# Kernel optimization log

Measured on AMD Instinct MI355X. Metric: run time of the kernel, lower is better.

## Reference

```python
import jax, jax.numpy as jnp
import numpy as np

B, S, E, D = 4, 4096, 512, 64

def setup_inputs() -> dict:
    key = jax.random.key(0)
    kx, kq, kk, kv = jax.random.split(key, 4)
    # xavier_normal std = sqrt(2/(E+D))
    std = float(np.sqrt(2.0 / (E + D)))
    return {
        "x": jax.random.normal(kx, (B, S, E), dtype=jnp.float32),
        "WQ": jax.random.normal(kq, (E, D), dtype=jnp.float32) * std,
        "WK": jax.random.normal(kk, (E, D), dtype=jnp.float32) * std,
        "WV": jax.random.normal(kv, (E, D), dtype=jnp.float32) * std,
    }

def reference(x, WQ, WK, WV):
    # Single-head causal attention; NOTE: scale uses embedding_size (E), as in source.
    Q = x @ WQ  # [B,S,D]
    K = x @ WK
    V = x @ WV
    scale = 1.0 / jnp.sqrt(jnp.float32(E))
    scores = jnp.einsum("bqd,bkd->bqk", Q, K) * scale  # [B,S,S]
    s = scores.shape[1]
    causal = jnp.tril(jnp.ones((s, s), dtype=bool))  # True = keep
    scores = jnp.where(causal[None, :, :], scores, -jnp.inf)
    attn = jax.nn.softmax(scores, axis=2)
    return jnp.einsum("bqk,bkd->bqd", attn, V)
```

## Files before the change

### kernel.cpp

```cpp
#include <hip/hip_runtime.h>
#include <hip/hip_bf16.h>

namespace {
constexpr int B = 4, S = 4096, E = 512, D = 64;
constexpr int CHUNK = 8;
constexpr float SCALE_LOG2E = 0.04419417382415922f * 1.4426950408889634f;

typedef __bf16 bf16x8 __attribute__((ext_vector_type(8)));
typedef float floatx4 __attribute__((ext_vector_type(4)));
}

__global__ __launch_bounds__(256) void prep_wt(
    const float* __restrict__ WQ, const float* __restrict__ WK,
    const float* __restrict__ WV, __bf16* __restrict__ Wt)
{
    __shared__ __bf16 tile[64][72];
    const int t = threadIdx.x;
    const int mat = blockIdx.x >> 3;
    const int k0  = (blockIdx.x & 7) * 64;
    const float* W = (mat == 0) ? WQ : (mat == 1) ? WK : WV;
    #pragma unroll
    for (int i = 0; i < 16; ++i) {
        const int k = (t >> 6) + i * 4;
        tile[t & 63][k] = (__bf16)W[(k0 + k) * 64 + (t & 63)];
    }
    __syncthreads();
    #pragma unroll
    for (int i = 0; i < 2; ++i) {
        const int u = t + 256 * i;
        const int n = u >> 3, kseg = (u & 7) * 8;
        *(bf16x8*)(Wt + (mat * 64 + n) * 512 + k0 + kseg) =
            *(const bf16x8*)&tile[n][kseg];
    }
}

__global__ __launch_bounds__(256) void qkv_mfma(
    const float* __restrict__ x, const __bf16* __restrict__ Wt,
    __bf16* __restrict__ Qb, __bf16* __restrict__ Kfrag,
    __bf16* __restrict__ Vfrag)
{
    __shared__ __bf16 xs[32][72];
    __shared__ __bf16 vsh[64][48];

    const int t = threadIdx.x;
    const int wave = t >> 6, lane = t & 63, quad = lane >> 4, l16 = lane & 15;
    const long row0 = (long)blockIdx.x * 32;
    const int xrr = t >> 3, xcc = (t & 7) * 8;

    const __bf16* wbase = Wt + (wave * 48 + l16) * 512 + quad * 8;

    floatx4 acc[2][3];
    #pragma unroll
    for (int m = 0; m < 2; ++m)
        #pragma unroll
        for (int n = 0; n < 3; ++n) acc[m][n] = (floatx4){0.f, 0.f, 0.f, 0.f};

    float4 xf0, xf1;
    bf16x8 wf[6];
    {
        const float* src = x + (row0 + xrr) * E + xcc;
        xf0 = *(const float4*)src;
        xf1 = *(const float4*)(src + 4);
        #pragma unroll
        for (int ns = 0; ns < 3; ++ns)
            #pragma unroll
            for (int ch = 0; ch < 2; ++ch)
                wf[ns * 2 + ch] = *(const bf16x8*)(wbase + ns * 16 * 512 + ch * 32);
    }

    #pragma unroll
    for (int kc = 0; kc < 8; ++kc) {
        __syncthreads();
        {
            bf16x8 v;
            v[0] = (__bf16)xf0.x; v[1] = (__bf16)xf0.y;
            v[2] = (__bf16)xf0.z; v[3] = (__bf16)xf0.w;
            v[4] = (__bf16)xf1.x; v[5] = (__bf16)xf1.y;
            v[6] = (__bf16)xf1.z; v[7] = (__bf16)xf1.w;
            *(bf16x8*)&xs[xrr][xcc] = v;
        }
        __syncthreads();

        bf16x8 wcur[6];
        #pragma unroll
        for (int i = 0; i < 6; ++i) wcur[i] = wf[i];

        if (kc < 7) {
            const float* src = x + (row0 + xrr) * E + (kc + 1) * 64 + xcc;
            xf0 = *(const float4*)src;
            xf1 = *(const float4*)(src + 4);
            #pragma unroll
            for (int ns = 0; ns < 3; ++ns)
                #pragma unroll
                for (int ch = 0; ch < 2; ++ch)
                    wf[ns * 2 + ch] =
                        *(const bf16x8*)(wbase + ns * 16 * 512 + (kc + 1) * 64 + ch * 32);
        }

        bf16x8 aa[2][2];
        #pragma unroll
        for (int m = 0; m < 2; ++m)
            #pragma unroll
            for (int ch = 0; ch < 2; ++ch)
                aa[m][ch] = *(const bf16x8*)&xs[m * 16 + l16][ch * 32 + quad * 8];
        #pragma unroll
        for (int ns = 0; ns < 3; ++ns) {
            #pragma unroll
            for (int ch = 0; ch < 2; ++ch) {
                #pragma unroll
                for (int m = 0; m < 2; ++m)
                    acc[m][ns] = __builtin_amdgcn_mfma_f32_16x16x32_bf16(
                        aa[m][ch], wcur[ns * 2 + ch], acc[m][ns], 0, 0, 0);
            }
        }
    }

    const long bb_ = row0 >> 12;
    const int s0 = (int)(row0 & 4095);
    const int kt = s0 >> 6;
    const int ch_tok = (s0 >> 5) & 1;
    const long kvobase = ((long)(bb_ * 64 + kt)) * 4096;

    #pragma unroll
    for (int ns = 0; ns < 3; ++ns) {
        const int g = wave * 3 + ns;
        const int mat = g >> 2;
        const int col = (g & 3) * 16 + l16;
        #pragma unroll
        for (int m = 0; m < 2; ++m) {
            if (mat == 0) {
                #pragma unroll
                for (int r = 0; r < 4; ++r)
                    Qb[(row0 + m * 16 + quad * 4 + r) * 64 + col] = (__bf16)acc[m][ns][r];
            } else if (mat == 1) {
                const int d  = col;
                const int ch = d >> 5, kq = (d & 31) >> 3, j = d & 7;
                const int sub = ch_tok * 2 + m;
                #pragma unroll
                for (int r = 0; r < 4; ++r) {
                    const int kl = quad * 4 + r;
                    Kfrag[kvobase + (sub * 2 + ch) * 512 + (kq * 16 + kl) * 8 + j]
                        = (__bf16)acc[m][ns][r];
                }
            } else {
                __bf16 p[4];
                #pragma unroll
                for (int r = 0; r < 4; ++r) p[r] = (__bf16)acc[m][ns][r];
                *(unsigned long long*)&vsh[col][m * 16 + quad * 4] =
                    *(unsigned long long*)p;
            }
        }
    }
    __syncthreads();
    {
        const int dsb = t >> 6, q = (t >> 4) & 3, dl = t & 15;
        bf16x8 v = *(const bf16x8*)&vsh[dsb * 16 + dl][q * 8];
        *(bf16x8*)(Vfrag + kvobase + (dsb * 2 + ch_tok) * 512 + (q * 16 + dl) * 8) = v;
    }
}

__global__ __launch_bounds__(256) void attn_kernel(
    const __bf16* __restrict__ Qg, const __bf16* __restrict__ Kfrag,
    const __bf16* __restrict__ Vfrag, __bf16* __restrict__ Opart,
    float* __restrict__ Lpart)
{
    __shared__ __bf16 Ps[4][16][72];

    int g = 287 - blockIdx.x;
    int a = 0;
    while (g >= 4 * (a + 1) * (a + 2)) ++a;
    const int rem = g - 4 * a * (a + 1);
    const int qt  = 8 * a + rem / (a + 1);
    const int c   = rem % (a + 1);

    const int b  = blockIdx.y;
    const int q0 = qt * 64;
    const int t  = threadIdx.x;
    const int wave = t >> 6, lane = t & 63, quad = lane >> 4, l16 = lane & 15;

    const int nkt    = qt + 1;
    const int kstart = c * CHUNK;
    const int kend   = min(kstart + CHUNK, nkt);

    const __bf16* qrow = Qg + ((long)(b * S + q0 + wave * 16 + l16)) * D;
    bf16x8 aq[2];
    aq[0] = *(const bf16x8*)(qrow + quad * 8);
    aq[1] = *(const bf16x8*)(qrow + 32 + quad * 8);

    bf16x8 ones;
    #pragma unroll
    for (int j = 0; j < 8; ++j) ones[j] = (__bf16)1.0f;

    floatx4 o[4];
    #pragma unroll
    for (int i = 0; i < 4; ++i) o[i] = (floatx4){0.f, 0.f, 0.f, 0.f};
    floatx4 lsum = (floatx4){0.f, 0.f, 0.f, 0.f};

    const __bf16* Kf_ = Kfrag + (long)b * 64 * 8 * 512 + lane * 8;
    const __bf16* Vf_ = Vfrag + (long)b * 64 * 8 * 512 + lane * 8;

    bf16x8 kf[4][2];
    #pragma unroll
    for (int ns = 0; ns < 4; ++ns)
        #pragma unroll
        for (int ch = 0; ch < 2; ++ch)
            kf[ns][ch] = *(const bf16x8*)(Kf_ + ((long)kstart * 8 + ns * 2 + ch) * 512);

    for (int ktg = kstart; ktg < kend; ++ktg) {
        bf16x8 vfr[4][2];
        #pragma unroll
        for (int dsb = 0; dsb < 4; ++dsb)
            #pragma unroll
            for (int ch = 0; ch < 2; ++ch)
                vfr[dsb][ch] = *(const bf16x8*)(Vf_ + ((long)ktg * 8 + dsb * 2 + ch) * 512);

        floatx4 sf[4];
        #pragma unroll
        for (int ns = 0; ns < 4; ++ns) {
            floatx4 cacc = (floatx4){0.f, 0.f, 0.f, 0.f};
            #pragma unroll
            for (int ch = 0; ch < 2; ++ch)
                cacc = __builtin_amdgcn_mfma_f32_16x16x32_bf16(
                    kf[ns][ch], aq[ch], cacc, 0, 0, 0);
            sf[ns] = cacc;
        }

        if (ktg + 1 < kend) {
            #pragma unroll
            for (int ns = 0; ns < 4; ++ns)
                #pragma unroll
                for (int ch = 0; ch < 2; ++ch)
                    kf[ns][ch] = *(const bf16x8*)(
                        Kf_ + ((long)(ktg + 1) * 8 + ns * 2 + ch) * 512);
        }

        if (ktg == nkt - 1) {
            const int q = q0 + wave * 16 + l16;
            const int kbase = ktg * 64;
            #pragma unroll
            for (int ns = 0; ns < 4; ++ns)
                #pragma unroll
                for (int r = 0; r < 4; ++r) {
                    const int key = kbase + ns * 16 + quad * 4 + r;
                    if (key > q) sf[ns][r] = -1e30f;
                }
        }

        #pragma unroll
        for (int ns = 0; ns < 4; ++ns) {
            __bf16 p4[4];
            #pragma unroll
            for (int r = 0; r < 4; ++r)
                p4[r] = (__bf16)__builtin_amdgcn_exp2f(sf[ns][r] * SCALE_LOG2E);
            *(unsigned long long*)&Ps[wave][l16][ns * 16 + quad * 4] =
                *(unsigned long long*)p4;
        }

        bf16x8 ap[2];
        ap[0] = *(const bf16x8*)&Ps[wave][l16][quad * 8];
        ap[1] = *(const bf16x8*)&Ps[wave][l16][32 + quad * 8];

        lsum = __builtin_amdgcn_mfma_f32_16x16x32_bf16(ones, ap[0], lsum, 0, 0, 0);
        lsum = __builtin_amdgcn_mfma_f32_16x16x32_bf16(ones, ap[1], lsum, 0, 0, 0);

        #pragma unroll
        for (int dsb = 0; dsb < 4; ++dsb) {
            floatx4 cacc = o[dsb];
            #pragma unroll
            for (int ch = 0; ch < 2; ++ch)
                cacc = __builtin_amdgcn_mfma_f32_16x16x32_bf16(
                    vfr[dsb][ch], ap[ch], cacc, 0, 0, 0);
            o[dsb] = cacc;
        }
    }

    const long rbase = (long)c * (B * S) + (long)b * S + q0 + wave * 16;
    #pragma unroll
    for (int dsb = 0; dsb < 4; ++dsb) {
        __bf16 p4[4];
        #pragma unroll
        for (int r = 0; r < 4; ++r) p4[r] = (__bf16)o[dsb][r];
        *(unsigned long long*)(Opart + (rbase + l16) * 64 + dsb * 16 + quad * 4) =
            *(unsigned long long*)p4;
    }
    if (quad == 0)
        Lpart[rbase + l16] = lsum[0];
}

__global__ __launch_bounds__(256) void combine_kernel(
    const __bf16* __restrict__ Opart, const float* __restrict__ Lpart,
    float* __restrict__ Og)
{
    const int idx = blockIdx.x * 256 + threadIdx.x;
    const int row = idx >> 3, seg = (idx & 7) * 8;
    const int qt = (row & (S - 1)) >> 6;
    const int nc = (qt >> 3) + 1;
    float acc[8] = {0, 0, 0, 0, 0, 0, 0, 0};
    float l = 0.f;
    for (int c = 0; c < nc; ++c) {
        bf16x8 ov = *(const bf16x8*)(Opart + ((long)c * (B * S) + row) * 64 + seg);
        l += Lpart[(long)c * (B * S) + row];
        #pragma unroll
        for (int j = 0; j < 8; ++j) acc[j] += (float)ov[j];
    }
    const float invl = 1.f / l;
    float* dst = Og + (long)row * 64 + seg;
    float4 o0 = {acc[0] * invl, acc[1] * invl, acc[2] * invl, acc[3] * invl};
    float4 o1 = {acc[4] * invl, acc[5] * invl, acc[6] * invl, acc[7] * invl};
    *(float4*)dst = o0;
    *(float4*)(dst + 4) = o1;
}

extern "C" void kernel_launch(void* const* d_in, const int* in_sizes, int n_in,
                              void* d_out, int out_size, void* d_ws, size_t ws_size,
                              hipStream_t stream)
{
    const float* x  = (const float*)d_in[0];
    const float* WQ = (const float*)d_in[1];
    const float* WK = (const float*)d_in[2];
    const float* WV = (const float*)d_in[3];
    float* out = (float*)d_out;

    __bf16* Qb = (__bf16*)d_ws;
    __bf16* Kfrag = Qb + (size_t)B * S * D;
    __bf16* Vfrag = Kfrag + (size_t)B * S * D;
    __bf16* Wt = Vfrag + (size_t)B * S * D;
    __bf16* Opart = Wt + (size_t)3 * E * D;
    float*  Lpart = (float*)(Opart + (size_t)8 * B * S * D);

    prep_wt<<<dim3(24), 256, 0, stream>>>(WQ, WK, WV, Wt);
    qkv_mfma<<<dim3((B * S) / 32), 256, 0, stream>>>(x, Wt, Qb, Kfrag, Vfrag);
    attn_kernel<<<dim3(288, B), 256, 0, stream>>>(Qb, Kfrag, Vfrag, Opart, Lpart);
    combine_kernel<<<dim3((B * S * 8) / 256), 256, 0, stream>>>(Opart, Lpart, out);
}
```

Measured before the change: 119.8 us.

## Process 128-query tiles per block so each wave reuses K/V fragments across two row groups

The attention kernel now handles 128 query rows per block, 32 per wave, instead of 64. Each K/V fragment loaded from global memory feeds two 16-row query groups, which halves K/V load traffic per query and doubles MFMA work per load. The block count halves and the chunk/tile mapping and combine kernel are adjusted to match. The cost is more registers per wave (two sets of accumulators and scores), extra causal waste for waves whose rows end before the last key tile, and fewer blocks for load balancing.

New measurement: 117.2 us. -2.2%, faster.

```diff
diff --git a/kernel.cpp b/kernel.cpp
--- a/kernel.cpp
+++ b/kernel.cpp
@@ -164,37 +164,43 @@
     const __bf16* __restrict__ Vfrag, __bf16* __restrict__ Opart,
     float* __restrict__ Lpart)
 {
-    __shared__ __bf16 Ps[4][16][72];
-
-    int g = 287 - blockIdx.x;
+    __shared__ __bf16 Ps[4][2][16][72];
+
+    int g = 143 - blockIdx.x;
     int a = 0;
-    while (g >= 4 * (a + 1) * (a + 2)) ++a;
-    const int rem = g - 4 * a * (a + 1);
-    const int qt  = 8 * a + rem / (a + 1);
+    while (g >= 2 * (a + 1) * (a + 2)) ++a;
+    const int rem = g - 2 * a * (a + 1);
+    const int qt2 = 4 * a + rem / (a + 1);
     const int c   = rem % (a + 1);
 
     const int b  = blockIdx.y;
-    const int q0 = qt * 64;
+    const int q0 = qt2 * 128;
     const int t  = threadIdx.x;
     const int wave = t >> 6, lane = t & 63, quad = lane >> 4, l16 = lane & 15;
 
-    const int nkt    = qt + 1;
+    const int nkt_w  = 2 * qt2 + 1 + (wave >> 1);
     const int kstart = c * CHUNK;
-    const int kend   = min(kstart + CHUNK, nkt);
-
-    const __bf16* qrow = Qg + ((long)(b * S + q0 + wave * 16 + l16)) * D;
-    bf16x8 aq[2];
-    aq[0] = *(const bf16x8*)(qrow + quad * 8);
-    aq[1] = *(const bf16x8*)(qrow + 32 + quad * 8);
+    const int kend   = min(kstart + CHUNK, nkt_w);
+
+    bf16x8 aq[2][2];
+    #pragma unroll
+    for (int qm = 0; qm < 2; ++qm) {
+        const __bf16* qrow =
+            Qg + ((long)(b * S + q0 + wave * 32 + qm * 16 + l16)) * D;
+        aq[qm][0] = *(const bf16x8*)(qrow + quad * 8);
+        aq[qm][1] = *(const bf16x8*)(qrow + 32 + quad * 8);
+    }
 
     bf16x8 ones;
     #pragma unroll
     for (int j = 0; j < 8; ++j) ones[j] = (__bf16)1.0f;
 
-    floatx4 o[4];
-    #pragma unroll
-    for (int i = 0; i < 4; ++i) o[i] = (floatx4){0.f, 0.f, 0.f, 0.f};
-    floatx4 lsum = (floatx4){0.f, 0.f, 0.f, 0.f};
+    floatx4 o[2][4];
+    #pragma unroll
+    for (int qm = 0; qm < 2; ++qm)
+        #pragma unroll
+        for (int i = 0; i < 4; ++i) o[qm][i] = (floatx4){0.f, 0.f, 0.f, 0.f};
+    floatx4 lsum[2] = {(floatx4){0.f, 0.f, 0.f, 0.f}, (floatx4){0.f, 0.f, 0.f, 0.f}};
 
     const __bf16* Kf_ = Kfrag + (long)b * 64 * 8 * 512 + lane * 8;
     const __bf16* Vf_ = Vfrag + (long)b * 64 * 8 * 512 + lane * 8;
@@ -207,6 +213,8 @@
             kf[ns][ch] = *(const bf16x8*)(Kf_ + ((long)kstart * 8 + ns * 2 + ch) * 512);
 
     for (int ktg = kstart; ktg < kend; ++ktg) {
+        const int kbase = ktg * 64;
+
         bf16x8 vfr[4][2];
         #pragma unroll
         for (int dsb = 0; dsb < 4; ++dsb)
@@ -214,16 +222,18 @@
             for (int ch = 0; ch < 2; ++ch)
                 vfr[dsb][ch] = *(const bf16x8*)(Vf_ + ((long)ktg * 8 + dsb * 2 + ch) * 512);
 
-        floatx4 sf[4];
-        #pragma unroll
-        for (int ns = 0; ns < 4; ++ns) {
-            floatx4 cacc = (floatx4){0.f, 0.f, 0.f, 0.f};
-            #pragma unroll
-            for (int ch = 0; ch < 2; ++ch)
-                cacc = __builtin_amdgcn_mfma_f32_16x16x32_bf16(
-                    kf[ns][ch], aq[ch], cacc, 0, 0, 0);
-            sf[ns] = cacc;
-        }
+        floatx4 sf[2][4];
+        #pragma unroll
+        for (int qm = 0; qm < 2; ++qm)
+            #pragma unroll
+            for (int ns = 0; ns < 4; ++ns) {
+                floatx4 cacc = (floatx4){0.f, 0.f, 0.f, 0.f};
+                #pragma unroll
+                for (int ch = 0; ch < 2; ++ch)
+                    cacc = __builtin_amdgcn_mfma_f32_16x16x32_bf16(
+                        kf[ns][ch], aq[qm][ch], cacc, 0, 0, 0);
+                sf[qm][ns] = cacc;
+            }
 
         if (ktg + 1 < kend) {
             #pragma unroll
@@ -234,57 +244,68 @@
                         Kf_ + ((long)(ktg + 1) * 8 + ns * 2 + ch) * 512);
         }
 
-        if (ktg == nkt - 1) {
-            const int q = q0 + wave * 16 + l16;
-            const int kbase = ktg * 64;
-            #pragma unroll
-            for (int ns = 0; ns < 4; ++ns)
-                #pragma unroll
-                for (int r = 0; r < 4; ++r) {
-                    const int key = kbase + ns * 16 + quad * 4 + r;
-                    if (key > q) sf[ns][r] = -1e30f;
-                }
-        }
-
-        #pragma unroll
-        for (int ns = 0; ns < 4; ++ns) {
+        #pragma unroll
+        for (int qm = 0; qm < 2; ++qm) {
+            const int qfb = q0 + wave * 32 + qm * 16;
+            if (kbase + 63 > qfb) {
+                const int q = qfb + l16;
+                #pragma unroll
+                for (int ns = 0; ns < 4; ++ns)
+                    #pragma unroll
+                    for (int r = 0; r < 4; ++r) {
+                        const int key = kbase + ns * 16 + quad * 4 + r;
+                        if (key > q) sf[qm][ns][r] = -1e30f;
+                    }
+            }
+        }
+
+        #pragma unroll
+        for (int qm = 0; qm < 2; ++qm)
+            #pragma unroll
+            for (int ns = 0; ns < 4; ++ns) {
+                __bf16 p4[4];
+                #pragma unroll
+                for (int r = 0; r < 4; ++r)
+                    p4[r] = (__bf16)__builtin_amdgcn_exp2f(sf[qm][ns][r] * SCALE_LOG2E);
+                *(unsigned long long*)&Ps[wave][qm][l16][ns * 16 + quad * 4] =
+                    *(unsigned long long*)p4;
+            }
+
+        #pragma unroll
+        for (int qm = 0; qm < 2; ++qm) {
+            bf16x8 ap[2];
+            ap[0] = *(const bf16x8*)&Ps[wave][qm][l16][quad * 8];
+            ap[1] = *(const bf16x8*)&Ps[wave][qm][l16][32 + quad * 8];
+
+            lsum[qm] = __builtin_amdgcn_mfma_f32_16x16x32_bf16(ones, ap[0], lsum[qm], 0, 0, 0);
+            lsum[qm] = __builtin_amdgcn_mfma_f32_16x16x32_bf16(ones, ap[1], lsum[qm], 0, 0, 0);
+
+            #pragma unroll
+            for (int dsb = 0; dsb < 4; ++dsb) {
+                floatx4 cacc = o[qm][dsb];
+                #pragma unroll
+                for (int ch = 0; ch < 2; ++ch)
+                    cacc = __builtin_amdgcn_mfma_f32_16x16x32_bf16(
+                        vfr[dsb][ch], ap[ch], cacc, 0, 0, 0);
+                o[qm][dsb] = cacc;
+            }
+        }
+    }
+
+    const long rbase = (long)c * (B * S) + (long)b * S + q0 + wave * 32;
+    #pragma unroll
+    for (int qm = 0; qm < 2; ++qm) {
+        #pragma unroll
+        for (int dsb = 0; dsb < 4; ++dsb) {
             __bf16 p4[4];
             #pragma unroll
-            for (int r = 0; r < 4; ++r)
-                p4[r] = (__bf16)__builtin_amdgcn_exp2f(sf[ns][r] * SCALE_LOG2E);
-            *(unsigned long long*)&Ps[wave][l16][ns * 16 + quad * 4] =
+            for (int r = 0; r < 4; ++r) p4[r] = (__bf16)o[qm][dsb][r];
+            *(unsigned long long*)(Opart + (rbase + qm * 16 + l16) * 64 + dsb * 16 + quad * 4) =
                 *(unsigned long long*)p4;
         }
-
-        bf16x8 ap[2];
-        ap[0] = *(const bf16x8*)&Ps[wave][l16][quad * 8];
-        ap[1] = *(const bf16x8*)&Ps[wave][l16][32 + quad * 8];
-
-        lsum = __builtin_amdgcn_mfma_f32_16x16x32_bf16(ones, ap[0], lsum, 0, 0, 0);
-        lsum = __builtin_amdgcn_mfma_f32_16x16x32_bf16(ones, ap[1], lsum, 0, 0, 0);
-
-        #pragma unroll
-        for (int dsb = 0; dsb < 4; ++dsb) {
-            floatx4 cacc = o[dsb];
-            #pragma unroll
-            for (int ch = 0; ch < 2; ++ch)
-                cacc = __builtin_amdgcn_mfma_f32_16x16x32_bf16(
-                    vfr[dsb][ch], ap[ch], cacc, 0, 0, 0);
-            o[dsb] = cacc;
-        }
-    }
-
-    const long rbase = (long)c * (B * S) + (long)b * S + q0 + wave * 16;
-    #pragma unroll
-    for (int dsb = 0; dsb < 4; ++dsb) {
-        __bf16 p4[4];
-        #pragma unroll
-        for (int r = 0; r < 4; ++r) p4[r] = (__bf16)o[dsb][r];
-        *(unsigned long long*)(Opart + (rbase + l16) * 64 + dsb * 16 + quad * 4) =
-            *(unsigned long long*)p4;
-    }
-    if (quad == 0)
-        Lpart[rbase + l16] = lsum[0];
+        if (quad == 0)
+            Lpart[rbase + qm * 16 + l16] = lsum[qm][0];
+    }
 }
 
 __global__ __launch_bounds__(256) void combine_kernel(
@@ -293,8 +314,8 @@
 {
     const int idx = blockIdx.x * 256 + threadIdx.x;
     const int row = idx >> 3, seg = (idx & 7) * 8;
-    const int qt = (row & (S - 1)) >> 6;
-    const int nc = (qt >> 3) + 1;
+    const int qt2 = (row & (S - 1)) >> 7;
+    const int nc = (qt2 >> 2) + 1;
     float acc[8] = {0, 0, 0, 0, 0, 0, 0, 0};
     float l = 0.f;
     for (int c = 0; c < nc; ++c) {
@@ -330,6 +351,6 @@
 
     prep_wt<<<dim3(24), 256, 0, stream>>>(WQ, WK, WV, Wt);
     qkv_mfma<<<dim3((B * S) / 32), 256, 0, stream>>>(x, Wt, Qb, Kfrag, Vfrag);
-    attn_kernel<<<dim3(288, B), 256, 0, stream>>>(Qb, Kfrag, Vfrag, Opart, Lpart);
+    attn_kernel<<<dim3(144, B), 256, 0, stream>>>(Qb, Kfrag, Vfrag, Opart, Lpart);
     combine_kernel<<<dim3((B * S * 8) / 256), 256, 0, stream>>>(Opart, Lpart, out);
 }
```
